# Kernel tuning notes

Hardware: AMD Instinct MI355X
Metric: run time of the kernel (lower is better)

Reference implementation:

```python
import jax, jax.numpy as jnp
import numpy as np

NUM_SELECT = 300
OUT_H = 448
OUT_W = 448


def setup_inputs() -> dict:
    key = jax.random.key(0)
    k1, k2, k3 = jax.random.split(key, 3)
    B, Q, C = 4, 900, 91
    pred_logits = jax.random.normal(k1, (B, Q, C), dtype=jnp.float32)
    pred_boxes = jax.random.uniform(k2, (B, Q, 4), dtype=jnp.float32)  # cxcywh in [0,1)
    pred_masks = jax.random.normal(k3, (B, Q, 28, 28), dtype=jnp.float32)
    # all images same size so resize output shape is static under jit
    target_sizes = jnp.full((B, 2), OUT_H, dtype=jnp.int64 if jax.config.jax_enable_x64 else jnp.int32)
    return {"pred_logits": pred_logits, "pred_boxes": pred_boxes,
            "pred_masks": pred_masks, "target_sizes": target_sizes}


def _box_cxcywh_to_xyxy(b):
    cx, cy, w, h = jnp.split(b, 4, axis=-1)
    return jnp.concatenate([cx - 0.5 * w, cy - 0.5 * h, cx + 0.5 * w, cy + 0.5 * h], axis=-1)


def reference(pred_logits, pred_boxes, pred_masks, target_sizes):
    B, Q, C = pred_logits.shape
    # sigmoid + topk over flattened (query, class) axis
    prob = jax.nn.sigmoid(pred_logits).reshape(B, Q * C)
    scores, topk_idx = jax.lax.top_k(prob, NUM_SELECT)          # [B, K]
    topk_boxes = topk_idx // C                                   # query index [B, K]
    labels = topk_idx % C                                        # class index [B, K]

    boxes = _box_cxcywh_to_xyxy(pred_boxes)                      # [B, Q, 4]
    boxes = jnp.take_along_axis(boxes, topk_boxes[:, :, None], axis=1)  # [B, K, 4]

    img_h = target_sizes[:, 0].astype(boxes.dtype)
    img_w = target_sizes[:, 1].astype(boxes.dtype)
    scale = jnp.stack([img_w, img_h, img_w, img_h], axis=1)      # [B, 4]
    boxes = boxes * scale[:, None, :]

    # gather top-k masks: [B, K, 28, 28]
    masks = jnp.take_along_axis(pred_masks, topk_boxes[:, :, None, None], axis=1)
    masks = masks.astype(jnp.float16)
    # bilinear, half-pixel centers == torch align_corners=False
    resize_one = lambda m: jax.image.resize(m, (NUM_SELECT, OUT_H, OUT_W), method="bilinear")
    masks = jax.vmap(resize_one)(masks)                          # [B, K, OUT_H, OUT_W] fp16

    return scores, labels, boxes, masks
```

## Files before the change

kernel.cpp:

```cpp
#include <hip/hip_runtime.h>
#include <hip/hip_fp16.h>

#define QN 900
#define CN 91
#define TOTN (QN * CN)
#define KSEL 300
#define BN 4
#define OUTW 448
#define MASKPIX (OUTW * OUTW)
#define OFFS_LABELS (BN * KSEL)
#define OFFS_BOXES  (2 * BN * KSEL)
#define OFFS_MASKS  (6 * BN * KSEL)
#define MAXC 2048
#define BT 1024

#define APB 4
#define AELEM (TOTN / APB)

typedef float floatx4 __attribute__((ext_vector_type(4)));

static __device__ __forceinline__ unsigned fkey(float f) {
    unsigned u = __float_as_uint(f);
    return (u & 0x80000000u) ? ~u : (u | 0x80000000u);
}

__global__ __launch_bounds__(1024) void hist_part(
    const float* __restrict__ logits, unsigned* __restrict__ wsh)
{
    const int b = blockIdx.x >> 2, part = blockIdx.x & 3;
    const int tid = threadIdx.x;
    const float* lg = logits + (size_t)b * TOTN + (size_t)part * AELEM;

    __shared__ unsigned h[256 * 9];
    for (int i = tid; i < 256 * 9; i += 1024) h[i] = 0;
    __syncthreads();
    const int sl = tid & 7;
    for (int i = tid; i < AELEM; i += 1024)
        atomicAdd(&h[(fkey(lg[i]) >> 24) * 9 + sl], 1u);
    __syncthreads();
    if (tid < 256) {
        unsigned s = 0;
#pragma unroll
        for (int k = 0; k < 8; ++k) s += h[tid * 9 + k];
        wsh[blockIdx.x * 256 + tid] = s;
    }
}

__global__ __launch_bounds__(BT) void select_final(
    const float* __restrict__ logits, const float* __restrict__ boxes,
    const int* __restrict__ tsz, const unsigned* __restrict__ wsh,
    float* out, int* qsel)
{
    const int b = blockIdx.x;
    const int tid = threadIdx.x;
    const float* lg = logits + (size_t)b * TOTN;

    __shared__ unsigned hist[256];
    __shared__ int sh_bin, sh_want, sh_chunk;
    __shared__ unsigned sh_above, sh_cnt;
    __shared__ int cidx[MAXC];
    __shared__ unsigned ckey[MAXC];

    if (tid < 256) {
        unsigned s = 0;
#pragma unroll
        for (int p = 0; p < APB; ++p) s += wsh[(b * APB + p) * 256 + tid];
        hist[tid] = s;
    }
    __syncthreads();

    unsigned prefix = 0;
    int want = KSEL;
#pragma unroll
    for (int round = 0; round < 2; ++round) {
        const int shift = 24 - 8 * round;
        if (round > 0) {
            if (tid < 256) hist[tid] = 0;
            __syncthreads();
            for (int i = tid; i < TOTN; i += BT) {
                unsigned key = fkey(lg[i]);
                if ((key & 0xFF000000u) == prefix)
                    atomicAdd(&hist[(key >> 16) & 255u], 1u);
            }
            __syncthreads();
        }
        if (tid < 64) {
            unsigned p = hist[tid * 4] + hist[tid * 4 + 1]
                       + hist[tid * 4 + 2] + hist[tid * 4 + 3];
            unsigned suffix = p;
#pragma unroll
            for (int o = 1; o < 64; o <<= 1) {
                unsigned t = __shfl_down(suffix, o);
                if (tid + o < 64) suffix += t;
            }
            unsigned nxt = __shfl_down(suffix, 1);
            if (tid == 63) nxt = 0;
            bool flag = (suffix >= (unsigned)want) && (nxt < (unsigned)want);
            if (flag) { sh_chunk = tid; sh_above = nxt; }
        }
        __syncthreads();
        if (tid == 0) {
            int ch = sh_chunk;
            unsigned acc = sh_above;
            int j = 3;
            for (; j > 0; --j) {
                if (acc + hist[ch * 4 + j] >= (unsigned)want) break;
                acc += hist[ch * 4 + j];
            }
            sh_bin = ch * 4 + j;
            sh_want = want - (int)acc;
        }
        __syncthreads();
        prefix |= ((unsigned)sh_bin << shift);
        want = sh_want;
        __syncthreads();
    }
    const unsigned T16 = prefix >> 16;

    if (tid == 0) sh_cnt = 0;
    __syncthreads();
    for (int i = tid; i < TOTN; i += BT) {
        unsigned key = fkey(lg[i]);
        if ((key >> 16) >= T16) {
            unsigned p = atomicAdd(&sh_cnt, 1u);
            if (p < MAXC) { cidx[p] = i; ckey[p] = key; }
        }
    }
    __syncthreads();
    const int ncand = min((int)sh_cnt, MAXC);

    const float fh = (float)tsz[b * 2 + 0];
    const float fw = (float)tsz[b * 2 + 1];

    for (int c = tid; c < ncand; c += BT) {
        const unsigned kc = ckey[c];
        const int ic = cidx[c];
        int rank = 0;
        for (int s = 0; s < ncand; ++s) {
            unsigned ks = ckey[s];
            if (ks > kc || (ks == kc && cidx[s] < ic)) ++rank;
        }
        if (rank < KSEL) {
            float lf = lg[ic];
            float score = 1.0f / (1.0f + expf(-lf));
            int q = ic / CN;
            int label = ic - q * CN;

            out[b * KSEL + rank] = score;
            out[OFFS_LABELS + b * KSEL + rank] = (float)label;

            const float* bx = boxes + ((size_t)b * QN + q) * 4;
            float cx = bx[0], cy = bx[1], ww = bx[2], hh = bx[3];
            float* ob = out + OFFS_BOXES + ((size_t)(b * KSEL + rank)) * 4;
            ob[0] = (cx - 0.5f * ww) * fw;
            ob[1] = (cy - 0.5f * hh) * fh;
            ob[2] = (cx + 0.5f * ww) * fw;
            ob[3] = (cy + 0.5f * hh) * fh;

            qsel[b * KSEL + rank] = q;
        }
    }
}

#define SPLIT 4
#define ROWSB (OUTW / SPLIT)

static __device__ __forceinline__ void mask_body(
    const float* __restrict__ masks, const int* __restrict__ qsel,
    float* __restrict__ out, int ebid)
{
    const int mk = ebid >> 2;
    const int part = ebid & 3;
    const int b = mk / KSEL;
    const int q = qsel[mk];
    const float* __restrict__ src = masks + ((size_t)b * QN + q) * 784;

    const int j = threadIdx.x & 127;
    const int rhalf = threadIdx.x >> 7;
    if (j >= 112) return;

    const int qd = j & 3;
    const int i4 = j >> 2;
    const int c0 = i4 - 1 + (qd >> 1);
    const int c0c = c0 < 0 ? 0 : c0;
    const int c1c = (c0 + 1 > 27) ? 27 : c0 + 1;
    const float toff = 0.25f * (float)qd - ((qd >= 2) ? 1.0f : 0.0f);
    const float t0 = 0.53125f + toff, t1 = 0.59375f + toff,
                t2 = 0.65625f + toff, t3 = 0.71875f + toff;

    const int ystart = part * ROWSB + rhalf;
    float* optr = out + OFFS_MASKS + (size_t)mk * MASKPIX
                + (size_t)ystart * OUTW + j * 4;

    float sy = (float)ystart * 0.0625f - 0.46875f;
    int prev_iy = -1000;
    float m00 = 0.f, m01 = 0.f, d0 = 0.f, d1 = 0.f;

#pragma unroll 2
    for (int k = 0; k < ROWSB / 2; ++k) {
        float yf = floorf(sy);
        float ty = sy - yf;
        int iy = (int)yf;
        if (iy != prev_iy) {
            prev_iy = iy;
            int y0 = iy < 0 ? 0 : iy;
            int y1 = (iy + 1 > 27) ? 27 : iy + 1;
            float a0 = src[y0 * 28 + c0c];
            float a1 = src[y0 * 28 + c1c];
            float b0 = src[y1 * 28 + c0c];
            float b1 = src[y1 * 28 + c1c];
            m00 = a0; m01 = a1;
            d0 = b0 - a0; d1 = b1 - a1;
        }
        float v0 = fmaf(ty, d0, m00);
        float v1 = fmaf(ty, d1, m01);
        float dv = v1 - v0;
        floatx4 w;
        w.x = fmaf(t0, dv, v0);
        w.y = fmaf(t1, dv, v0);
        w.z = fmaf(t2, dv, v0);
        w.w = fmaf(t3, dv, v0);
        *reinterpret_cast<floatx4*>(optr) = w;
        optr += 2 * OUTW;
        sy += 0.125f;
    }
}

__global__ __launch_bounds__(256) void mask_kernel_swz(
    const float* __restrict__ masks, const int* __restrict__ qsel,
    float* __restrict__ out)
{
    const int ebid = (blockIdx.x & 7) * 600 + (blockIdx.x >> 3);
    mask_body(masks, qsel, out, ebid);
}

extern "C" void kernel_launch(void* const* d_in, const int* in_sizes, int n_in,
                              void* d_out, int out_size, void* d_ws, size_t ws_size,
                              hipStream_t stream) {
    const float* pred_logits = (const float*)d_in[0];
    const float* pred_boxes  = (const float*)d_in[1];
    const float* pred_masks  = (const float*)d_in[2];
    const int*   target_sz   = (const int*)d_in[3];
    float* out = (float*)d_out;
    int* qsel = (int*)d_ws;
    unsigned* wsh = (unsigned*)((char*)d_ws + 5120);

    hist_part<<<BN * APB, 1024, 0, stream>>>(pred_logits, wsh);
    select_final<<<BN, BT, 0, stream>>>(pred_logits, pred_boxes, target_sz,
                                        wsh, out, qsel);
    mask_kernel_swz<<<BN * KSEL * SPLIT, 256, 0, stream>>>(pred_masks, qsel, out);
}
```

Before: 253.7 us.

## Split top-k selection into parallel 8-bit threshold gather and rank kernels

Replaces the single-block-per-batch select kernel, which did a second histogram pass plus a candidate scan over all logits, with a multi-block gather kernel. It uses only the first 8-bit histogram threshold and appends candidates to a global buffer through global atomics. A separate rank kernel loads the candidates into shared memory, ranks them by pairwise comparison, and recovers the logit from the key. This spreads the logit scans across 32 blocks instead of 4 and drops one full pass. The coarser threshold yields more candidates, capped at 3072, which makes the quadratic ranking costlier and could silently drop candidates if more exceed the cap.

```diff
diff --git a/kernel.cpp b/kernel.cpp
--- a/kernel.cpp
+++ b/kernel.cpp
@@ -11,11 +11,17 @@
 #define OFFS_LABELS (BN * KSEL)
 #define OFFS_BOXES  (2 * BN * KSEL)
 #define OFFS_MASKS  (6 * BN * KSEL)
-#define MAXC 2048
-#define BT 1024
 
 #define APB 4
 #define AELEM (TOTN / APB)
+#define GPB 8
+#define GSL 10238
+#define NCMAX 3072
+
+#define QSEL_OFF 0
+#define WSH_OFF  5120
+#define CNT_OFF  22528
+#define CAND_OFF 24576
 
 typedef float floatx4 __attribute__((ext_vector_type(4)));
 
@@ -25,11 +31,14 @@
 }
 
 __global__ __launch_bounds__(1024) void hist_part(
-    const float* __restrict__ logits, unsigned* __restrict__ wsh)
+    const float* __restrict__ logits, unsigned* __restrict__ wsh,
+    unsigned* __restrict__ cnt)
 {
     const int b = blockIdx.x >> 2, part = blockIdx.x & 3;
     const int tid = threadIdx.x;
     const float* lg = logits + (size_t)b * TOTN + (size_t)part * AELEM;
+
+    if (blockIdx.x == 0 && tid < BN) cnt[tid] = 0;
 
     __shared__ unsigned h[256 * 9];
     for (int i = tid; i < 256 * 9; i += 1024) h[i] = 0;
@@ -46,20 +55,15 @@
     }
 }
 
-__global__ __launch_bounds__(BT) void select_final(
-    const float* __restrict__ logits, const float* __restrict__ boxes,
-    const int* __restrict__ tsz, const unsigned* __restrict__ wsh,
-    float* out, int* qsel)
-{
-    const int b = blockIdx.x;
+__global__ __launch_bounds__(1024) void gather_k(
+    const float* __restrict__ logits, const unsigned* __restrict__ wsh,
+    unsigned* __restrict__ cnt, uint2* __restrict__ cand)
+{
+    const int b = blockIdx.x >> 3, p8 = blockIdx.x & 7;
     const int tid = threadIdx.x;
-    const float* lg = logits + (size_t)b * TOTN;
 
     __shared__ unsigned hist[256];
-    __shared__ int sh_bin, sh_want, sh_chunk;
-    __shared__ unsigned sh_above, sh_cnt;
-    __shared__ int cidx[MAXC];
-    __shared__ unsigned ckey[MAXC];
+    __shared__ unsigned sh_t8;
 
     if (tid < 256) {
         unsigned s = 0;
@@ -68,80 +72,59 @@
         hist[tid] = s;
     }
     __syncthreads();
-
-    unsigned prefix = 0;
-    int want = KSEL;
-#pragma unroll
-    for (int round = 0; round < 2; ++round) {
-        const int shift = 24 - 8 * round;
-        if (round > 0) {
-            if (tid < 256) hist[tid] = 0;
-            __syncthreads();
-            for (int i = tid; i < TOTN; i += BT) {
-                unsigned key = fkey(lg[i]);
-                if ((key & 0xFF000000u) == prefix)
-                    atomicAdd(&hist[(key >> 16) & 255u], 1u);
-            }
-            __syncthreads();
-        }
-        if (tid < 64) {
-            unsigned p = hist[tid * 4] + hist[tid * 4 + 1]
-                       + hist[tid * 4 + 2] + hist[tid * 4 + 3];
-            unsigned suffix = p;
-#pragma unroll
-            for (int o = 1; o < 64; o <<= 1) {
-                unsigned t = __shfl_down(suffix, o);
-                if (tid + o < 64) suffix += t;
-            }
-            unsigned nxt = __shfl_down(suffix, 1);
-            if (tid == 63) nxt = 0;
-            bool flag = (suffix >= (unsigned)want) && (nxt < (unsigned)want);
-            if (flag) { sh_chunk = tid; sh_above = nxt; }
-        }
-        __syncthreads();
-        if (tid == 0) {
-            int ch = sh_chunk;
-            unsigned acc = sh_above;
-            int j = 3;
-            for (; j > 0; --j) {
-                if (acc + hist[ch * 4 + j] >= (unsigned)want) break;
-                acc += hist[ch * 4 + j];
-            }
-            sh_bin = ch * 4 + j;
-            sh_want = want - (int)acc;
-        }
-        __syncthreads();
-        prefix |= ((unsigned)sh_bin << shift);
-        want = sh_want;
-        __syncthreads();
-    }
-    const unsigned T16 = prefix >> 16;
-
-    if (tid == 0) sh_cnt = 0;
-    __syncthreads();
-    for (int i = tid; i < TOTN; i += BT) {
+    if (tid == 0) {
+        unsigned acc = 0;
+        int bin = 255;
+        for (; bin > 0; --bin) { acc += hist[bin]; if (acc >= KSEL) break; }
+        sh_t8 = (unsigned)bin;
+    }
+    __syncthreads();
+    const unsigned T8 = sh_t8;
+
+    const float* lg = logits + (size_t)b * TOTN;
+    const int start = p8 * GSL;
+    const int end = min(start + GSL, TOTN);
+    for (int i = start + tid; i < end; i += 1024) {
         unsigned key = fkey(lg[i]);
-        if ((key >> 16) >= T16) {
-            unsigned p = atomicAdd(&sh_cnt, 1u);
-            if (p < MAXC) { cidx[p] = i; ckey[p] = key; }
-        }
-    }
-    __syncthreads();
-    const int ncand = min((int)sh_cnt, MAXC);
+        if ((key >> 24) >= T8) {
+            unsigned pos = atomicAdd(&cnt[b], 1u);
+            if (pos < NCMAX) cand[b * NCMAX + pos] = make_uint2(key, (unsigned)i);
+        }
+    }
+}
+
+__global__ __launch_bounds__(1024) void rank_emit(
+    const float* __restrict__ boxes, const int* __restrict__ tsz,
+    const unsigned* __restrict__ cnt, const uint2* __restrict__ cand,
+    float* out, int* __restrict__ qsel)
+{
+    const int b = blockIdx.x;
+    const int tid = threadIdx.x;
+
+    __shared__ unsigned lkey[NCMAX];
+    __shared__ int lidx[NCMAX];
+
+    const int ncand = min((int)cnt[b], NCMAX);
+    for (int i = tid; i < ncand; i += 1024) {
+        uint2 v = cand[b * NCMAX + i];
+        lkey[i] = v.x; lidx[i] = (int)v.y;
+    }
+    __syncthreads();
 
     const float fh = (float)tsz[b * 2 + 0];
     const float fw = (float)tsz[b * 2 + 1];
 
-    for (int c = tid; c < ncand; c += BT) {
-        const unsigned kc = ckey[c];
-        const int ic = cidx[c];
+    for (int c = tid; c < ncand; c += 1024) {
+        const unsigned kc = lkey[c];
+        const int ic = lidx[c];
         int rank = 0;
         for (int s = 0; s < ncand; ++s) {
-            unsigned ks = ckey[s];
-            if (ks > kc || (ks == kc && cidx[s] < ic)) ++rank;
+            unsigned ks = lkey[s];
+            rank += (ks > kc) ? 1 : ((ks == kc && lidx[s] < ic) ? 1 : 0);
         }
         if (rank < KSEL) {
-            float lf = lg[ic];
+            unsigned u = (kc & 0x80000000u) ? (kc & 0x7FFFFFFFu) : ~kc;
+            float lf = __uint_as_float(u);
             float score = 1.0f / (1.0f + expf(-lf));
             int q = ic / CN;
             int label = ic - q * CN;
@@ -242,11 +225,13 @@
     const float* pred_masks  = (const float*)d_in[2];
     const int*   target_sz   = (const int*)d_in[3];
     float* out = (float*)d_out;
-    int* qsel = (int*)d_ws;
-    unsigned* wsh = (unsigned*)((char*)d_ws + 5120);
-
-    hist_part<<<BN * APB, 1024, 0, stream>>>(pred_logits, wsh);
-    select_final<<<BN, BT, 0, stream>>>(pred_logits, pred_boxes, target_sz,
-                                        wsh, out, qsel);
+    int* qsel = (int*)((char*)d_ws + QSEL_OFF);
+    unsigned* wsh = (unsigned*)((char*)d_ws + WSH_OFF);
+    unsigned* cnt = (unsigned*)((char*)d_ws + CNT_OFF);
+    uint2* cand = (uint2*)((char*)d_ws + CAND_OFF);
+
+    hist_part<<<BN * APB, 1024, 0, stream>>>(pred_logits, wsh, cnt);
+    gather_k<<<BN * GPB, 1024, 0, stream>>>(pred_logits, wsh, cnt, cand);
+    rank_emit<<<BN, 1024, 0, stream>>>(pred_boxes, target_sz, cnt, cand, out, qsel);
     mask_kernel_swz<<<BN * KSEL * SPLIT, 256, 0, stream>>>(pred_masks, qsel, out);
 }
```

Result: slower. 392.5 us (+54.7%).
